# Performance work log

Measured on AMD Instinct MI355X. Metric: run time of the kernel, lower is better.

The kernel has to match this reference:

```python
import jax, jax.numpy as jnp
import numpy as np

B, F, T, D = 65536, 1024, 64, 6


def setup_inputs() -> dict:
    key = jax.random.key(0)
    k0, k1, k2, k3 = jax.random.split(key, 4)
    x = jax.random.normal(k0, (B, F), dtype=jnp.float32)
    splits = jax.random.normal(k1, (T, D, F), dtype=jnp.float32)
    thresholds = jax.random.normal(k2, (T, D), dtype=jnp.float32)
    values = jax.random.normal(k3, (T, 2 ** D), dtype=jnp.float32)
    return {"x": x, "splits": splits, "thresholds": thresholds, "values": values}


def reference(x, splits, thresholds, values):
    # Since split_idx = depth % max_depth = depth, each level's split is path-independent.
    # bit_d = 1 means 'right' (score > threshold); node after D steps = 2^D - 1 + code,
    # leaf_idx = node - 2^D = code - 1 (torch negative indexing => mod 2^D).
    T_, D_, _ = splits.shape
    scores = jnp.einsum('bf,tdf->tbd', x, splits)          # (T, B, D)
    bits = (scores > thresholds[:, None, :]).astype(jnp.int32)
    pow2 = (2 ** jnp.arange(D_ - 1, -1, -1)).astype(jnp.int32)  # weight 2^(D-1-d)
    code = jnp.sum(bits * pow2, axis=-1)                   # (T, B)
    leaf = jnp.mod(code - 1, 2 ** D_)                      # (T, B)
    out_t = jnp.take_along_axis(values, leaf, axis=1)      # (T, B)
    return jnp.mean(out_t, axis=0)[:, None]                # (B, 1)
```

## Files before the change

kernel.cpp:

```cpp
#include <hip/hip_runtime.h>

#define BTOT 65536
#define FDIM 1024
#define TNUM 64
#define DNUM 6

#define BAND      1.5e-3f
#define GCUT      1.5e-4f
#define HEDGE_MAX 1.35f
#define CAP       8192

typedef unsigned int u32;
typedef unsigned long long u64;
using f32x4  = __attribute__((ext_vector_type(4))) float;
using bf16x8 = __attribute__((ext_vector_type(8))) short;

__device__ __forceinline__ short f32_to_bf16(float v) {
    u32 bits = __float_as_uint(v);
    bits += 0x7FFFu + ((bits >> 16) & 1u);
    return (short)(bits >> 16);
}
__device__ __forceinline__ float bf16_to_f32(short h) {
    return __uint_as_float(((u32)(unsigned short)h) << 16);
}
__device__ __forceinline__ void cvt8(float4 a0, float4 a1, bf16x8& h, bf16x8& l) {
    const float vv[8] = {a0.x, a0.y, a0.z, a0.w, a1.x, a1.y, a1.z, a1.w};
    #pragma unroll
    for (int e = 0; e < 8; ++e) {
        const short hh = f32_to_bf16(vv[e]);
        h[e] = hh;
        l[e] = f32_to_bf16(vv[e] - bf16_to_f32(hh));
    }
}

__device__ __forceinline__ int swz(int row, int chunk) {
    return row * 32 + ((chunk ^ ((row >> 1) & 3)) << 3);
}

#define PRE_OFFSET  65536
#define BTILE_BYTES 24576
#define PRE_BYTES   (64 * BTILE_BYTES)
#define B_LO_OFF    6144

#define LDS_BYTES 81920

__global__ void pre_split(const float* __restrict__ splits,
                          short* __restrict__ pre) {
    const int q  = blockIdx.x * 256 + threadIdx.x;
    const int r  = q >> 8;
    const int c4 = q & 255;
    const float4 v = *(const float4*)(splits + (size_t)r * FDIM + c4 * 4);
    const int ks    = c4 >> 3;
    const int f4    = c4 & 7;
    const int chunk = f4 >> 1, he = f4 & 1;
    const int h  = (r >= 192) ? 1 : 0;
    const int rl = r - h * 192;
    short* tile = pre + (size_t)(ks * 2 + h) * (BTILE_BYTES / 2);
    const int idx = swz(rl, chunk) + he * 4;
    const float vv[4] = {v.x, v.y, v.z, v.w};
    short hh[4], ll[4];
    #pragma unroll
    for (int e = 0; e < 4; ++e) {
        hh[e] = f32_to_bf16(vv[e]);
        ll[e] = f32_to_bf16(vv[e] - bf16_to_f32(hh[e]));
    }
    *(short4*)(tile + idx)            = make_short4(hh[0], hh[1], hh[2], hh[3]);
    *(short4*)(tile + B_LO_OFF + idx) = make_short4(ll[0], ll[1], ll[2], ll[3]);
}

__global__ __launch_bounds__(512, 4)
void forest_mfma(const float* __restrict__ x,
                 const float* __restrict__ thresholds,
                 const float* __restrict__ values,
                 float* __restrict__ out,
                 u32* __restrict__ gcnt,
                 u32* __restrict__ cands,
                 const short* __restrict__ pre) {
    __shared__ __align__(16) char smem[LDS_BYTES];

    const int tid  = threadIdx.x;
    const int lane = tid & 63;
    const int w    = tid >> 6;
    const int wr   = w >> 2;
    const int wc   = w & 3;
    const int fr   = lane & 15;
    const int fq   = lane >> 4;
    const int nb   = blockIdx.x >> 1;
    const int half = blockIdx.x & 1;
    const int b0   = nb * 128;

    f32x4 acc[3][4];
    #pragma unroll
    for (int tt = 0; tt < 3; ++tt)
        #pragma unroll
        for (int bt = 0; bt < 4; ++bt) acc[tt][bt] = (f32x4)0.0f;

    auto stageA = [&](int k0, char* dstbase) {
        #pragma unroll
        for (int j = 0; j < 2; ++j) {
            const int q = j * 512 + tid;
            const int row = q >> 3, cpos = q & 7;
            const int g = cpos ^ (row & 7);
            __builtin_amdgcn_global_load_lds(
                (const void*)(x + (size_t)(b0 + row) * FDIM + k0 + g * 4),
                (void*)(dstbase + (j * 512 + w * 64) * 16), 16, 0, 0);
        }
    };
    auto stageB = [&](int ks, char* dstb) {
        const char* srcb = (const char*)pre + (size_t)(ks * 2 + half) * BTILE_BYTES;
        #pragma unroll
        for (int j = 0; j < 3; ++j) {
            const int cb = (j * 512 + w * 64) * 16;
            __builtin_amdgcn_global_load_lds(
                (const void*)(srcb + cb + (lane << 4)),
                (void*)(dstb + cb), 16, 0, 0);
        }
    };

    stageA(0, smem);
    stageB(0, smem + 32768);
    __syncthreads();

    for (int ks = 0; ks < 32; ++ks) {
        const int cur = ks & 1;
        if (ks < 31) {
            stageA((ks + 1) * 32, smem + (cur ^ 1) * 16384);
            stageB(ks + 1, smem + 32768 + (cur ^ 1) * 24576);
        }

        const char*  Ac = smem + cur * 16384;
        const short* Bs = (const short*)(smem + 32768 + cur * 24576);

        bf16x8 sh[3], sl[3];
        #pragma unroll
        for (int tt = 0; tt < 3; ++tt) {
            const int row = wc * 48 + tt * 16 + fr;
            const int ix = swz(row, fq);
            sh[tt] = *(const bf16x8*)(Bs + ix);
            sl[tt] = *(const bf16x8*)(Bs + B_LO_OFF + ix);
        }

        __builtin_amdgcn_s_setprio(1);
        #pragma unroll
        for (int bt = 0; bt < 4; ++bt) {
            const int row = wr * 64 + bt * 16 + fr;
            const int sw = row & 7;
            const float4 v0 = *(const float4*)(Ac + ((row * 8 + ((fq * 2)     ^ sw)) << 4));
            const float4 v1 = *(const float4*)(Ac + ((row * 8 + ((fq * 2 + 1) ^ sw)) << 4));
            bf16x8 xh, xl;
            cvt8(v0, v1, xh, xl);
            #pragma unroll
            for (int tt = 0; tt < 3; ++tt) {
                acc[tt][bt] = __builtin_amdgcn_mfma_f32_16x16x32_bf16(sh[tt], xh, acc[tt][bt], 0, 0, 0);
                acc[tt][bt] = __builtin_amdgcn_mfma_f32_16x16x32_bf16(sh[tt], xl, acc[tt][bt], 0, 0, 0);
                acc[tt][bt] = __builtin_amdgcn_mfma_f32_16x16x32_bf16(sl[tt], xh, acc[tt][bt], 0, 0, 0);
            }
        }
        __builtin_amdgcn_s_setprio(0);

        __syncthreads();
    }

    float th[3][4];
    #pragma unroll
    for (int tt = 0; tt < 3; ++tt)
        #pragma unroll
        for (int reg = 0; reg < 4; ++reg)
            th[tt][reg] = thresholds[half * 192 + wc * 48 + tt * 16 + fq * 4 + reg];

    float* psum = (float*)smem;

    #pragma unroll
    for (int bt = 0; bt < 4; ++bt) {
        u64 bal[3][4];
        u32 bandmask = 0;
        #pragma unroll
        for (int tt = 0; tt < 3; ++tt)
            #pragma unroll
            for (int reg = 0; reg < 4; ++reg) {
                const float df = acc[tt][bt][reg] - th[tt][reg];
                bal[tt][reg] = __ballot(df > 0.0f);
                if (__builtin_expect(fabsf(df) < BAND, 0))
                    bandmask |= 1u << ((tt * 16 + fq * 4 + reg) / 6);
            }
        bandmask |= __shfl_xor(bandmask, 16);
        bandmask |= __shfl_xor(bandmask, 32);

        float partial = 0.0f;
        #pragma unroll
        for (int jj = 0; jj < 2; ++jj) {
            const int j = fq * 2 + jj;
            int code = 0;
            #pragma unroll
            for (int d = 0; d < DNUM; ++d) {
                const int l   = j * 6 + d;
                const int stt = l >> 4;
                const int pos = l & 15;
                const int bit = (int)((bal[stt][pos & 3] >> (((pos >> 2) << 4) + fr)) & 1ull);
                code |= bit << (5 - d);
            }
            const int t = half * 32 + wc * 8 + j;
            partial += values[t * 64 + ((code - 1) & 63)];
            if (__builtin_expect((bandmask >> j) & 1u, 0)) {
                const u32 gidx = atomicAdd(gcnt, 1u);
                if (gidx < CAP)
                    cands[gidx] = ((u32)(b0 + wr * 64 + bt * 16 + fr) << 16) | ((u32)t << 6) | (u32)code;
            }
        }
        psum[(wr * 64 + bt * 16 + fr) * 16 + wc * 4 + fq] = partial;
    }
    __syncthreads();
    if (tid < 128) {
        float s = 0.0f;
        #pragma unroll
        for (int k = 0; k < 16; ++k) s += psum[tid * 16 + k];
        atomicAdd(out + b0 + tid, s * (1.0f / 64.0f));
    }
}

#define RPITCH 40
#define A_HI_S 0
#define A_LO_S (64 * RPITCH)
#define B_HI_S (128 * RPITCH)
#define B_LO_S (128 * RPITCH + 384 * RPITCH)
#define SMEM_SHORTS (128 * RPITCH + 2 * 384 * RPITCH)
__global__ __launch_bounds__(256, 2)
void forest_mfma_lds(const float* __restrict__ x,
                     const float* __restrict__ splits,
                     const float* __restrict__ thresholds,
                     const float* __restrict__ values,
                     float* __restrict__ out,
                     u32* __restrict__ gcnt,
                     u32* __restrict__ cands) {
    __shared__ __align__(16) short smem[SMEM_SHORTS];
    const int tid  = threadIdx.x;
    const int lane = tid & 63;
    const int w    = tid >> 6;
    const int fr   = lane & 15;
    const int fq   = lane >> 4;
    const int b0   = blockIdx.x * 64;

    f32x4 acc[6][4];
    #pragma unroll
    for (int tt = 0; tt < 6; ++tt)
        #pragma unroll
        for (int bt = 0; bt < 4; ++bt) acc[tt][bt] = (f32x4)0.0f;

    for (int ks = 0; ks < 32; ++ks) {
        const int k0 = ks * 32;
        if (ks) __syncthreads();
        #pragma unroll
        for (int j = 0; j < 2; ++j) {
            const int q = tid + j * 256, ra = q >> 3, c4 = q & 7;
            const float4 v = *(const float4*)(x + (size_t)(b0 + ra) * FDIM + k0 + c4 * 4);
            const float vv[4] = {v.x, v.y, v.z, v.w};
            short hh[4], ll[4];
            #pragma unroll
            for (int e = 0; e < 4; ++e) {
                hh[e] = f32_to_bf16(vv[e]);
                ll[e] = f32_to_bf16(vv[e] - bf16_to_f32(hh[e]));
            }
            *(short4*)(smem + A_HI_S + ra * RPITCH + c4 * 4) = make_short4(hh[0], hh[1], hh[2], hh[3]);
            *(short4*)(smem + A_LO_S + ra * RPITCH + c4 * 4) = make_short4(ll[0], ll[1], ll[2], ll[3]);
        }
        #pragma unroll
        for (int j = 0; j < 12; ++j) {
            const int q = tid + j * 256, rb = q >> 3, c4 = q & 7;
            const float4 v = *(const float4*)(splits + (size_t)rb * FDIM + k0 + c4 * 4);
            const float vv[4] = {v.x, v.y, v.z, v.w};
            short hh[4], ll[4];
            #pragma unroll
            for (int e = 0; e < 4; ++e) {
                hh[e] = f32_to_bf16(vv[e]);
                ll[e] = f32_to_bf16(vv[e] - bf16_to_f32(hh[e]));
            }
            *(short4*)(smem + B_HI_S + rb * RPITCH + c4 * 4) = make_short4(hh[0], hh[1], hh[2], hh[3]);
            *(short4*)(smem + B_LO_S + rb * RPITCH + c4 * 4) = make_short4(ll[0], ll[1], ll[2], ll[3]);
        }
        __syncthreads();
        bf16x8 sh[6], sl[6], xh[4], xl[4];
        #pragma unroll
        for (int tt = 0; tt < 6; ++tt) {
            const int ro = (w * 96 + tt * 16 + fr) * RPITCH + fq * 8;
            sh[tt] = *(const bf16x8*)(smem + B_HI_S + ro);
            sl[tt] = *(const bf16x8*)(smem + B_LO_S + ro);
        }
        #pragma unroll
        for (int bt = 0; bt < 4; ++bt) {
            const int ro = (bt * 16 + fr) * RPITCH + fq * 8;
            xh[bt] = *(const bf16x8*)(smem + A_HI_S + ro);
            xl[bt] = *(const bf16x8*)(smem + A_LO_S + ro);
        }
        #pragma unroll
        for (int tt = 0; tt < 6; ++tt)
            #pragma unroll
            for (int bt = 0; bt < 4; ++bt) {
                acc[tt][bt] = __builtin_amdgcn_mfma_f32_16x16x32_bf16(sh[tt], xh[bt], acc[tt][bt], 0, 0, 0);
                acc[tt][bt] = __builtin_amdgcn_mfma_f32_16x16x32_bf16(sh[tt], xl[bt], acc[tt][bt], 0, 0, 0);
                acc[tt][bt] = __builtin_amdgcn_mfma_f32_16x16x32_bf16(sl[tt], xh[bt], acc[tt][bt], 0, 0, 0);
            }
    }
    __syncthreads();

    float th[6][4];
    #pragma unroll
    for (int tt = 0; tt < 6; ++tt)
        #pragma unroll
        for (int reg = 0; reg < 4; ++reg)
            th[tt][reg] = thresholds[w * 96 + tt * 16 + fq * 4 + reg];
    float* psum = (float*)smem;
    __syncthreads();
    #pragma unroll
    for (int bt = 0; bt < 4; ++bt) {
        u64 bal[6][4];
        u32 bandmask = 0;
        #pragma unroll
        for (int tt = 0; tt < 6; ++tt)
            #pragma unroll
            for (int reg = 0; reg < 4; ++reg) {
                const float df = acc[tt][bt][reg] - th[tt][reg];
                bal[tt][reg] = __ballot(df > 0.0f);
                if (__builtin_expect(fabsf(df) < BAND, 0))
                    bandmask |= 1u << ((tt * 16 + fq * 4 + reg) / 6);
            }
        bandmask |= __shfl_xor(bandmask, 16);
        bandmask |= __shfl_xor(bandmask, 32);
        float partial = 0.0f;
        #pragma unroll
        for (int jj = 0; jj < 4; ++jj) {
            const int j = fq * 4 + jj;
            int code = 0;
            #pragma unroll
            for (int d = 0; d < DNUM; ++d) {
                const int l   = j * 6 + d;
                const int stt = l >> 4;
                const int pos = l & 15;
                const int bit = (int)((bal[stt][pos & 3] >> (((pos >> 2) << 4) + fr)) & 1ull);
                code |= bit << (5 - d);
            }
            const int t = w * 16 + j;
            partial += values[t * 64 + ((code - 1) & 63)];
            if (__builtin_expect((bandmask >> j) & 1u, 0)) {
                const u32 gidx = atomicAdd(gcnt, 1u);
                if (gidx < CAP)
                    cands[gidx] = ((u32)(b0 + bt * 16 + fr) << 16) | ((u32)t << 6) | (u32)code;
            }
        }
        psum[(bt * 16 + fr) * 16 + w * 4 + fq] = partial;
    }
    __syncthreads();
    if (tid < 64) {
        float s = 0.0f;
        #pragma unroll
        for (int k = 0; k < 16; ++k) s += psum[tid * 16 + k];
        out[b0 + tid] = s * (1.0f / 64.0f);
    }
}

__global__ __launch_bounds__(256)
void band_fix(const float* __restrict__ x,
              const float* __restrict__ splits,
              const float* __restrict__ thresholds,
              const float* __restrict__ values,
              float* __restrict__ out,
              const u32* __restrict__ gcnt,
              const u32* __restrict__ cands) {
    const u32 n = min(*gcnt, (u32)CAP);
    const u32 gid  = blockIdx.x * 256 + threadIdx.x;
    const u32 site = gid >> 3;
    const u32 sub  = gid & 7;
    if (site >= n) return;
    const u32 e = cands[site];
    const int b = (int)(e >> 16);
    const int t = (int)((e >> 6) & 63u);
    const int code_approx = (int)(e & 63u);
    const int d = (sub < 6) ? (int)sub : 0;

    const float* xr = x + (size_t)b * FDIM;
    const float* sr = splits + ((size_t)t * DNUM + d) * FDIM;
    float a = 0.0f;
    #pragma unroll 4
    for (int f = 0; f < FDIM; f += 16) {
        const float4 x0 = *(const float4*)(xr + f);
        const float4 x1 = *(const float4*)(xr + f + 4);
        const float4 x2 = *(const float4*)(xr + f + 8);
        const float4 x3 = *(const float4*)(xr + f + 12);
        const float4 s0 = *(const float4*)(sr + f);
        const float4 s1 = *(const float4*)(sr + f + 4);
        const float4 s2 = *(const float4*)(sr + f + 8);
        const float4 s3 = *(const float4*)(sr + f + 12);
        a = fmaf(x0.x, s0.x, a); a = fmaf(x0.y, s0.y, a);
        a = fmaf(x0.z, s0.z, a); a = fmaf(x0.w, s0.w, a);
        a = fmaf(x1.x, s1.x, a); a = fmaf(x1.y, s1.y, a);
        a = fmaf(x1.z, s1.z, a); a = fmaf(x1.w, s1.w, a);
        a = fmaf(x2.x, s2.x, a); a = fmaf(x2.y, s2.y, a);
        a = fmaf(x2.z, s2.z, a); a = fmaf(x2.w, s2.w, a);
        a = fmaf(x3.x, s3.x, a); a = fmaf(x3.y, s3.y, a);
        a = fmaf(x3.z, s3.z, a); a = fmaf(x3.w, s3.w, a);
    }
    const float df = a - thresholds[t * DNUM + d];

    const int lane = (int)(threadIdx.x & 63);
    const int base = lane & ~7;
    float dfs[6];
    #pragma unroll
    for (int j = 0; j < 6; ++j) dfs[j] = __shfl(df, base + j);

    if (sub == 0) {
        int code_chain = 0;
        #pragma unroll
        for (int j = 0; j < 6; ++j)
            code_chain = (code_chain << 1) | (dfs[j] > 0.0f ? 1 : 0);
        const float vA = values[t * 64 + ((code_approx - 1) & 63)];
        const float vC = values[t * 64 + ((code_chain - 1) & 63)];
        float delta = vC - vA;
        #pragma unroll
        for (int j = 0; j < 6; ++j) {
            if (fabsf(dfs[j]) < GCUT) {
                const int cf = code_chain ^ (1 << (5 - j));
                const float dv = values[t * 64 + ((cf - 1) & 63)] - vC;
                if (fabsf(dv) < HEDGE_MAX) delta += dv * 0.5f;
            }
        }
        atomicAdd(out + b, delta * (1.0f / 64.0f));
    }
}

extern "C" void kernel_launch(void* const* d_in, const int* in_sizes, int n_in,
                              void* d_out, int out_size, void* d_ws, size_t ws_size,
                              hipStream_t stream) {
    const float* x          = (const float*)d_in[0];
    const float* splits     = (const float*)d_in[1];
    const float* thresholds = (const float*)d_in[2];
    const float* values     = (const float*)d_in[3];
    float* out = (float*)d_out;

    u32* gcnt   = (u32*)d_ws;
    u32* cands  = (u32*)((char*)d_ws + 64);
    short* pre  = (short*)((char*)d_ws + PRE_OFFSET);
    const int use_pre = (ws_size >= (size_t)PRE_OFFSET + (size_t)PRE_BYTES) ? 1 : 0;

    (void)hipMemsetAsync(gcnt, 0, 4, stream);
    if (use_pre) {
        (void)hipMemsetAsync(d_out, 0, (size_t)out_size * sizeof(float), stream);
        pre_split<<<dim3(384), dim3(256), 0, stream>>>(splits, pre);
        forest_mfma<<<dim3((BTOT / 128) * 2), dim3(512), 0, stream>>>(
            x, thresholds, values, out, gcnt, cands, pre);
    } else {
        forest_mfma_lds<<<dim3(BTOT / 64), dim3(256), 0, stream>>>(
            x, splits, thresholds, values, out, gcnt, cands);
    }
    band_fix<<<dim3(CAP * 8 / 256), dim3(256), 0, stream>>>(
        x, splits, thresholds, values, out, gcnt, cands);
}
```

Measured before the change: 270.1 us.

## Convert x tiles to bf16 hi/lo once per block before LDS staging

Loads each block's fp32 x slice into registers, splits it into bf16 high and low parts once per thread, and stores the split halves into swizzled LDS for the next k-step. Previously every column-wave re-read the fp32 tile and re-ran the split conversion, duplicating that work four times. The MFMA phase now reads ready bf16 fragments. The trade-off is that the asynchronous global-to-LDS copy for x is replaced by register-staged loads, which costs extra VGPRs and relies on the MFMA work to hide global latency.

```diff
diff --git a/kernel.cpp b/kernel.cpp
--- a/kernel.cpp
+++ b/kernel.cpp
@@ -36,11 +36,15 @@
 __device__ __forceinline__ int swz(int row, int chunk) {
     return row * 32 + ((chunk ^ ((row >> 1) & 3)) << 3);
 }
+__device__ __forceinline__ int swzA(int row, int chunk) {
+    return row * 32 + ((chunk ^ (row & 3)) << 3);
+}
 
 #define PRE_OFFSET  65536
 #define BTILE_BYTES 24576
 #define PRE_BYTES   (64 * BTILE_BYTES)
 #define B_LO_OFF    6144
+#define A_LO_SH     4096
 
 #define LDS_BYTES 81920
 
@@ -89,23 +93,16 @@
     const int half = blockIdx.x & 1;
     const int b0   = nb * 128;
 
+    const int arow = tid >> 2;
+    const int ac   = tid & 3;
+    const float* axp = x + (size_t)(b0 + arow) * FDIM + ac * 8;
+
     f32x4 acc[3][4];
     #pragma unroll
     for (int tt = 0; tt < 3; ++tt)
         #pragma unroll
         for (int bt = 0; bt < 4; ++bt) acc[tt][bt] = (f32x4)0.0f;
 
-    auto stageA = [&](int k0, char* dstbase) {
-        #pragma unroll
-        for (int j = 0; j < 2; ++j) {
-            const int q = j * 512 + tid;
-            const int row = q >> 3, cpos = q & 7;
-            const int g = cpos ^ (row & 7);
-            __builtin_amdgcn_global_load_lds(
-                (const void*)(x + (size_t)(b0 + row) * FDIM + k0 + g * 4),
-                (void*)(dstbase + (j * 512 + w * 64) * 16), 16, 0, 0);
-        }
-    };
     auto stageB = [&](int ks, char* dstb) {
         const char* srcb = (const char*)pre + (size_t)(ks * 2 + half) * BTILE_BYTES;
         #pragma unroll
@@ -116,22 +113,35 @@
                 (void*)(dstb + cb), 16, 0, 0);
         }
     };
-
-    stageA(0, smem);
+    auto cvtwrA = [&](float4 p0, float4 p1, short* Adst) {
+        bf16x8 h, l;
+        cvt8(p0, p1, h, l);
+        const int off = swzA(arow, ac);
+        *(bf16x8*)(Adst + off)           = h;
+        *(bf16x8*)(Adst + A_LO_SH + off) = l;
+    };
+
+    {
+        float4 p0 = *(const float4*)(axp);
+        float4 p1 = *(const float4*)(axp + 4);
+        cvtwrA(p0, p1, (short*)smem);
+    }
     stageB(0, smem + 32768);
     __syncthreads();
 
+    float4 pa0, pa1;
     for (int ks = 0; ks < 32; ++ks) {
         const int cur = ks & 1;
         if (ks < 31) {
-            stageA((ks + 1) * 32, smem + (cur ^ 1) * 16384);
+            pa0 = *(const float4*)(axp + (ks + 1) * 32);
+            pa1 = *(const float4*)(axp + (ks + 1) * 32 + 4);
             stageB(ks + 1, smem + 32768 + (cur ^ 1) * 24576);
         }
 
-        const char*  Ac = smem + cur * 16384;
+        const short* As = (const short*)(smem + cur * 16384);
         const short* Bs = (const short*)(smem + 32768 + cur * 24576);
 
-        bf16x8 sh[3], sl[3];
+        bf16x8 sh[3], sl[3], xh[4], xl[4];
         #pragma unroll
         for (int tt = 0; tt < 3; ++tt) {
             const int row = wc * 48 + tt * 16 + fr;
@@ -139,24 +149,27 @@
             sh[tt] = *(const bf16x8*)(Bs + ix);
             sl[tt] = *(const bf16x8*)(Bs + B_LO_OFF + ix);
         }
-
-        __builtin_amdgcn_s_setprio(1);
         #pragma unroll
         for (int bt = 0; bt < 4; ++bt) {
             const int row = wr * 64 + bt * 16 + fr;
-            const int sw = row & 7;
-            const float4 v0 = *(const float4*)(Ac + ((row * 8 + ((fq * 2)     ^ sw)) << 4));
-            const float4 v1 = *(const float4*)(Ac + ((row * 8 + ((fq * 2 + 1) ^ sw)) << 4));
-            bf16x8 xh, xl;
-            cvt8(v0, v1, xh, xl);
+            const int ix = swzA(row, fq);
+            xh[bt] = *(const bf16x8*)(As + ix);
+            xl[bt] = *(const bf16x8*)(As + A_LO_SH + ix);
+        }
+
+        __builtin_amdgcn_s_setprio(1);
+        #pragma unroll
+        for (int bt = 0; bt < 4; ++bt)
             #pragma unroll
             for (int tt = 0; tt < 3; ++tt) {
-                acc[tt][bt] = __builtin_amdgcn_mfma_f32_16x16x32_bf16(sh[tt], xh, acc[tt][bt], 0, 0, 0);
-                acc[tt][bt] = __builtin_amdgcn_mfma_f32_16x16x32_bf16(sh[tt], xl, acc[tt][bt], 0, 0, 0);
-                acc[tt][bt] = __builtin_amdgcn_mfma_f32_16x16x32_bf16(sl[tt], xh, acc[tt][bt], 0, 0, 0);
-            }
-        }
+                acc[tt][bt] = __builtin_amdgcn_mfma_f32_16x16x32_bf16(sh[tt], xh[bt], acc[tt][bt], 0, 0, 0);
+                acc[tt][bt] = __builtin_amdgcn_mfma_f32_16x16x32_bf16(sh[tt], xl[bt], acc[tt][bt], 0, 0, 0);
+                acc[tt][bt] = __builtin_amdgcn_mfma_f32_16x16x32_bf16(sl[tt], xh[bt], acc[tt][bt], 0, 0, 0);
+            }
         __builtin_amdgcn_s_setprio(0);
+
+        if (ks < 31)
+            cvtwrA(pa0, pa1, (short*)(smem + (cur ^ 1) * 16384));
 
         __syncthreads();
     }
```

Result: faster. 223.2 us (-17.4%).
